# Kernel tuning notes

Measured on AMD Instinct MI355X. Metric: run time of the kernel, lower is better.

Reference implementation:

```python
import jax, jax.numpy as jnp
import numpy as np

B, S, DIM, HD = 4, 1024, 2048, 128
H = DIM // HD  # 16 heads
GN_EPS = 1e-3  # Keras GroupNormalization default epsilon


def setup_inputs() -> dict:
    key = jax.random.key(0)
    ks = jax.random.split(key, 8)
    x = jax.random.normal(ks[0], (B, S, DIM), dtype=jnp.float32)
    k = jax.random.normal(ks[1], (B, S, DIM), dtype=jnp.float32)
    v = jax.random.normal(ks[2], (B, S, DIM), dtype=jnp.float32)
    # One shared QKV projection weight per head (dict.fromkeys bug in source
    # makes Q, K, V use the SAME Dense layer). Keras Dense: y = x @ W, W:(in,out)
    Wh = jax.random.normal(ks[3], (H, HD, HD), dtype=jnp.float32) / np.sqrt(HD)
    wg_w = jax.random.normal(ks[4], (DIM, DIM), dtype=jnp.float32) / np.sqrt(DIM)
    wo_w = jax.random.normal(ks[5], (DIM, DIM), dtype=jnp.float32) / np.sqrt(DIM)
    gn_gamma = jnp.ones((DIM,), dtype=jnp.float32)
    gn_beta = jnp.zeros((DIM,), dtype=jnp.float32)
    return {"x": x, "k": k, "v": v, "Wh": Wh, "wg_w": wg_w, "wo_w": wo_w,
            "gn_gamma": gn_gamma, "gn_beta": gn_beta}


def _decay_masks(n_heads, seq_len):
    # Source: band_part(gamma**(i-j), 0, -1) then transpose ->
    # D[h, i, j] = gamma_h ** (j - i) for j <= i, else 0.
    gam = 1.0 - 2.0 ** (-5.0 - jnp.arange(n_heads, dtype=jnp.float32))  # (H,)
    idx = jnp.arange(seq_len, dtype=jnp.float32)
    expo = idx[None, :] - idx[:, None]               # (S,S): j - i
    D = jnp.where(expo[None, :, :] <= 0,
                  gam[:, None, None] ** expo[None, :, :], 0.0)  # (H,S,S)
    # TF: D /= reduce_sum(D, 1)**0.5 broadcasts row-sums along the COLUMN axis
    return D / jnp.sqrt(D.sum(axis=-1))[:, None, :]


def reference(x, k, v, Wh, wg_w, wo_w, gn_gamma, gn_beta):
    b, s, dim = x.shape
    h, hd, _ = Wh.shape
    # split last axis into contiguous per-head chunks
    xh = x.reshape(b, s, h, hd)
    kh = k.reshape(b, s, h, hd)
    vh = v.reshape(b, s, h, hd)
    # Q, K, V share the same per-head weight (faithful to dict.fromkeys)
    Q = jnp.einsum('bshd,hde->bshe', xh, Wh)
    K = jnp.einsum('bshd,hde->bshe', kh, Wh)
    V = jnp.einsum('bshd,hde->bshe', vh, Wh)
    scores = jnp.einsum('bshe,bthe->bhst', Q, K) / jnp.sqrt(jnp.float32(hd))
    Dn = _decay_masks(h, s)                          # (H,S,S)
    masked = scores * Dn[None, :, :, :]              # (B,H,S,S)
    # source reduces over axis 0 == BATCH, then abs, then clamp at 1
    A = jnp.maximum(jnp.abs(masked.sum(axis=0)), 1.0)  # (H,S,S)
    O = jnp.einsum('hst,bthe->bshe', A, V).reshape(b, s, dim)
    # GroupNormalization(groups=1): per-token layernorm over channels
    mu = O.mean(axis=-1, keepdims=True)
    var = O.var(axis=-1, keepdims=True)
    Y = (O - mu) / jnp.sqrt(var + GN_EPS) * gn_gamma + gn_beta
    W = jax.nn.relu(x @ wg_w)                        # gated branch
    return (W * Y) @ wo_w
```

## Files before the change

### kernel.cpp

```cpp
#include <hip/hip_runtime.h>
#include <math.h>

constexpr int Bc = 4, Sc = 1024, Dc = 2048, HDc = 128, Hc = 16;
constexpr int BSc = Bc * Sc;
constexpr int KQKc = Bc * HDc;
#define GN_EPS 1e-3f

typedef __bf16 bf16x8 __attribute__((ext_vector_type(8)));
typedef __bf16 bf16x4 __attribute__((ext_vector_type(4)));
typedef float f32x4 __attribute__((ext_vector_type(4)));

constexpr size_t OFF_Q   = 0;
constexpr size_t OFF_K   = OFF_Q + (size_t)Hc * Sc * KQKc / 2;
constexpr size_t OFF_VB  = OFF_K + (size_t)Hc * Sc * KQKc / 2;
constexpr size_t OFF_VT  = OFF_VB + (size_t)BSc * Dc / 2;
constexpr size_t OFF_A   = OFF_VT + (size_t)BSc * Dc / 2;
constexpr size_t OFF_O   = OFF_A + (size_t)Hc * Sc * Sc / 2;
constexpr size_t OFF_CT  = OFF_O + (size_t)BSc * Dc;
constexpr size_t OFF_PN  = OFF_CT + (size_t)Hc * Sc;
constexpr size_t OFF_XB  = OFF_PN + (size_t)Hc * Sc;
constexpr size_t OFF_WGT = OFF_XB + (size_t)BSc * Dc / 2;
constexpr size_t OFF_WOT = OFF_WGT + (size_t)Dc * Dc / 2;
constexpr size_t OFF_SUF = OFF_WOT + (size_t)Dc * Dc / 2;
constexpr size_t OFF_T   = OFF_SUF + (size_t)64 * 9 * HDc;
constexpr size_t OFF_WHT = OFF_T + (size_t)64 * 8 * HDc;
constexpr size_t OFF_KB2 = OFF_A;
constexpr size_t OFF_VB2 = OFF_A + (size_t)BSc * Dc / 2;

#define GLOAD_LDS16(gp, lp)                                               \
  __builtin_amdgcn_global_load_lds(                                       \
      (const __attribute__((address_space(1))) void*)(gp),                \
      (__attribute__((address_space(3))) void*)(lp), 16, 0, 0)


__global__ __launch_bounds__(256) void k_tables(float* __restrict__ ct,
                                                float* __restrict__ pn) {
  int idx = blockIdx.x * 256 + threadIdx.x;
  int h = idx >> 10, t = idx & 1023;
  double gamma = 1.0 - exp2(-(double)(5 + h));
  double l2g = log2(gamma);
  double r = 1.0 / gamma;
  double rowsum = (exp2(-(double)(t + 1) * l2g) - 1.0) / (r - 1.0);
  ct[idx] = (float)(exp2((double)t * l2g) / sqrt(rowsum));
  pn[idx] = (float)exp2(-(double)t * l2g);
}

__global__ __launch_bounds__(256) void k_cast83(const float* __restrict__ s0,
                                                const float* __restrict__ s1,
                                                const float* __restrict__ s2,
                                                __bf16* __restrict__ d0,
                                                __bf16* __restrict__ d1,
                                                __bf16* __restrict__ d2) {
  const int y = blockIdx.y;
  const float* src = (y == 0) ? s0 : (y == 1) ? s1 : s2;
  __bf16* dst = (y == 0) ? d0 : (y == 1) ? d1 : d2;
  size_t i = ((size_t)blockIdx.x * 256 + threadIdx.x) * 8;
  float4 a = *(const float4*)(src + i);
  float4 b = *(const float4*)(src + i + 4);
  bf16x8 o;
  o[0] = (__bf16)a.x; o[1] = (__bf16)a.y; o[2] = (__bf16)a.z; o[3] = (__bf16)a.w;
  o[4] = (__bf16)b.x; o[5] = (__bf16)b.y; o[6] = (__bf16)b.z; o[7] = (__bf16)b.w;
  *(bf16x8*)(dst + i) = o;
}

__global__ __launch_bounds__(256) void k_castT(const float* __restrict__ src,
                                               __bf16* __restrict__ dst) {
  __shared__ float t[32][33];
  const int bx = blockIdx.x, by = blockIdx.y;
  const int tid = threadIdx.x;
  const int lx = tid & 31, ly = tid >> 5;
  #pragma unroll
  for (int r = 0; r < 32; r += 8)
    t[ly + r][lx] = src[(size_t)(by * 32 + ly + r) * Dc + bx * 32 + lx];
  __syncthreads();
  #pragma unroll
  for (int r = 0; r < 32; r += 8)
    dst[(size_t)(bx * 32 + ly + r) * Dc + by * 32 + lx] = (__bf16)t[lx][ly + r];
}

__global__ __launch_bounds__(256) void k_whT(const float* __restrict__ Wh,
                                             __bf16* __restrict__ WhT) {
  __shared__ float t[32][33];
  const int h = blockIdx.z;
  const int d0 = blockIdx.x * 32, e0 = blockIdx.y * 32;
  const int tid = threadIdx.x;
  const int lx = tid & 31, ly = tid >> 5;
  #pragma unroll
  for (int r = 0; r < 32; r += 8)
    t[ly + r][lx] = Wh[(size_t)h * HDc * HDc + (d0 + ly + r) * HDc + e0 + lx];
  __syncthreads();
  #pragma unroll
  for (int r = 0; r < 32; r += 8)
    WhT[(size_t)h * HDc * HDc + (e0 + ly + r) * HDc + d0 + lx] =
        (__bf16)t[lx][ly + r];
}

__global__ __launch_bounds__(512) void k_projm(const __bf16* __restrict__ Xb,
                                               const __bf16* __restrict__ Kb2,
                                               const __bf16* __restrict__ Vb2,
                                               const __bf16* __restrict__ WhT,
                                               __bf16* __restrict__ Qo,
                                               __bf16* __restrict__ Ko,
                                               __bf16* __restrict__ Vo) {
  const int r0 = blockIdx.x * 128;
  const int h = blockIdx.y;
  const int z = blockIdx.z;
  const __bf16* src = (z == 0) ? Xb : (z == 1) ? Kb2 : Vb2;
  __shared__ __bf16 As[128 * 32];
  __shared__ __bf16 Bs[128 * 32];
  const int tid = threadIdx.x;
  const int wave = tid >> 6, lane = tid & 63;
  const int wm = (wave >> 2) * 64, wn = (wave & 3) * 32;
  const int grow = wave * 16 + (lane >> 2);
  const int gkb = ((lane & 3) ^ ((lane >> 3) & 3)) * 8;
  const int rl = lane & 15, kq = lane >> 4;
  const int sw8 = (kq ^ ((rl >> 1) & 3)) * 8;
  const int cha = wm >> 4, chb = wn >> 4;
  const __bf16* wb = WhT + (size_t)h * HDc * HDc;
  f32x4 acc[4][2] = {{}};
  for (int k0 = 0; k0 < HDc; k0 += 32) {
    GLOAD_LDS16(src + (size_t)(r0 + grow) * Dc + h * HDc + k0 + gkb,
                As + wave * 512);
    GLOAD_LDS16(wb + (size_t)grow * HDc + k0 + gkb, Bs + wave * 512);
    __syncthreads();
    bf16x8 a[4], b[2];
    #pragma unroll
    for (int i = 0; i < 4; ++i)
      a[i] = *(const bf16x8*)&As[(cha + i) * 512 + rl * 32 + sw8];
    #pragma unroll
    for (int j = 0; j < 2; ++j)
      b[j] = *(const bf16x8*)&Bs[(chb + j) * 512 + rl * 32 + sw8];
    #pragma unroll
    for (int i = 0; i < 4; ++i)
      #pragma unroll
      for (int j = 0; j < 2; ++j)
        acc[i][j] = __builtin_amdgcn_mfma_f32_16x16x32_bf16(a[i], b[j],
                                                            acc[i][j], 0, 0, 0);
    __syncthreads();
  }
  #pragma unroll
  for (int i = 0; i < 4; ++i) {
    #pragma unroll
    for (int j = 0; j < 2; ++j) {
      const int col = wn + j * 16 + rl;
      #pragma unroll
      for (int r = 0; r < 4; ++r) {
        const int row = r0 + wm + i * 16 + kq * 4 + r;
        const __bf16 v = (__bf16)acc[i][j][r];
        if (z == 2) {
          Vo[(size_t)row * Dc + h * HDc + col] = v;
        } else {
          const int s = row & 1023, bb = row >> 10;
          __bf16* dst = (z == 0) ? Qo : Ko;
          dst[((size_t)(h * Sc + s) * Bc + bb) * HDc + col] = v;
        }
      }
    }
  }
}

__global__ __launch_bounds__(256) void k_vt(const __bf16* __restrict__ VB,
                                            __bf16* __restrict__ Vt) {
  __shared__ float tl[32][33];
  const int bh = blockIdx.z, bb = bh >> 4, h = bh & 15;
  const int t0 = blockIdx.x * 32, e0 = blockIdx.y * 32;
  const int tid = threadIdx.x;
  const int lx = tid & 31, ly = tid >> 5;
  #pragma unroll
  for (int r = 0; r < 32; r += 8)
    tl[ly + r][lx] =
        (float)VB[(size_t)(bb * Sc + t0 + ly + r) * Dc + h * HDc + e0 + lx];
  __syncthreads();
  #pragma unroll
  for (int r = 0; r < 32; r += 8)
    Vt[((size_t)bh * HDc + e0 + ly + r) * Sc + t0 + lx] = (__bf16)tl[lx][ly + r];
}

__global__ __launch_bounds__(256) void k_vsum(const __bf16* __restrict__ VB,
                                              float* __restrict__ T) {
  const int jj = blockIdx.x, bh = blockIdx.y;
  const int bb = bh >> 4, h = bh & 15;
  const int tid = threadIdx.x;
  const int tp = tid >> 7, e = tid & 127;
  const __bf16* base =
      VB + (size_t)(bb * Sc + jj * 128 + tp * 64) * Dc + h * HDc + e;
  float a0 = 0.f, a1 = 0.f, a2 = 0.f, a3 = 0.f;
  float a4 = 0.f, a5 = 0.f, a6 = 0.f, a7 = 0.f;
  for (int t = 0; t < 64; t += 8) {
    a0 += (float)base[(size_t)(t + 0) * Dc];
    a1 += (float)base[(size_t)(t + 1) * Dc];
    a2 += (float)base[(size_t)(t + 2) * Dc];
    a3 += (float)base[(size_t)(t + 3) * Dc];
    a4 += (float)base[(size_t)(t + 4) * Dc];
    a5 += (float)base[(size_t)(t + 5) * Dc];
    a6 += (float)base[(size_t)(t + 6) * Dc];
    a7 += (float)base[(size_t)(t + 7) * Dc];
  }
  const float s = ((a0 + a1) + (a2 + a3)) + ((a4 + a5) + (a6 + a7));
  __shared__ float red[2][128];
  red[tp][e] = s;
  __syncthreads();
  if (tp == 0)
    T[((size_t)bh * 8 + jj) * HDc + e] = red[0][e] + red[1][e];
}

__global__ __launch_bounds__(128) void k_vscan(const float* __restrict__ T,
                                               float* __restrict__ SufV) {
  const int bh = blockIdx.x;
  const int e = threadIdx.x;
  float acc = 0.f;
  SufV[((size_t)bh * 9 + 8) * HDc + e] = 0.f;
  for (int jj = 7; jj >= 1; --jj) {
    acc += T[((size_t)bh * 8 + jj) * HDc + e];
    SufV[((size_t)bh * 9 + jj) * HDc + e] = acc;
  }
}

__global__ __launch_bounds__(512) void k_ssm(const __bf16* __restrict__ Q,
                                             const __bf16* __restrict__ Kb,
                                             const float* __restrict__ ct,
                                             const float* __restrict__ pn,
                                             __bf16* __restrict__ A) {
  const int bx = blockIdx.x, by = blockIdx.y;
  if (bx > by) return;
  const int h = blockIdx.z;
  const int t0 = bx * 128, s0 = by * 128;
  const int tid = threadIdx.x;
  __bf16* Ah = A + (size_t)h * Sc * Sc;
  __shared__ __bf16 Qs[128 * 32];
  __shared__ __bf16 Ks[128 * 32];
  const int wave = tid >> 6, lane = tid & 63;
  const int wm = (wave >> 2) * 64, wn = (wave & 3) * 32;
  const int grow = wave * 16 + (lane >> 2);
  const int gkb = ((lane & 3) ^ ((lane >> 3) & 3)) * 8;
  const int rl = lane & 15, kq = lane >> 4;
  const int sw8 = (kq ^ ((rl >> 1) & 3)) * 8;
  const int cha = wm >> 4, chb = wn >> 4;
  f32x4 acc[4][2] = {{}};
  const __bf16* qbase = Q + (size_t)(h * Sc + s0) * KQKc;
  const __bf16* kbase = Kb + (size_t)(h * Sc + t0) * KQKc;
  for (int k0 = 0; k0 < KQKc; k0 += 32) {
    GLOAD_LDS16(qbase + (size_t)grow * KQKc + k0 + gkb, Qs + wave * 512);
    GLOAD_LDS16(kbase + (size_t)grow * KQKc + k0 + gkb, Ks + wave * 512);
    __syncthreads();
    bf16x8 a[4], b[2];
    #pragma unroll
    for (int i = 0; i < 4; ++i)
      a[i] = *(const bf16x8*)&Qs[(cha + i) * 512 + rl * 32 + sw8];
    #pragma unroll
    for (int j = 0; j < 2; ++j)
      b[j] = *(const bf16x8*)&Ks[(chb + j) * 512 + rl * 32 + sw8];
    #pragma unroll
    for (int i = 0; i < 4; ++i)
      #pragma unroll
      for (int j = 0; j < 2; ++j)
        acc[i][j] = __builtin_amdgcn_mfma_f32_16x16x32_bf16(a[i], b[j],
                                                            acc[i][j], 0, 0, 0);
    __syncthreads();
  }
  const float rs = 0.088388347648318447f;
  #pragma unroll
  for (int i = 0; i < 4; ++i) {
    #pragma unroll
    for (int j = 0; j < 2; ++j) {
      const int t = t0 + wn + j * 16 + rl;
      const float ctv = ct[h * Sc + t] * rs;
      #pragma unroll
      for (int r = 0; r < 4; ++r) {
        const int s = s0 + wm + i * 16 + kq * 4 + r;
        float v = 1.0f;
        if (t <= s) v = fmaxf(fabsf(ctv * pn[h * Sc + s] * acc[i][j][r]), 1.0f);
        Ah[(size_t)s * Sc + t] = (__bf16)v;
      }
    }
  }
}

__global__ __launch_bounds__(512) void k_avm(const __bf16* __restrict__ A,
                                             const __bf16* __restrict__ Vt,
                                             const float* __restrict__ SufV,
                                             float* __restrict__ O) {
  const int bh = blockIdx.z, bb = bh >> 4, h = bh & 15;
  const int itile = blockIdx.x;
  const int s0 = itile * 128;
  const int tid = threadIdx.x;
  __shared__ __bf16 As[128 * 32];
  __shared__ __bf16 Bs[128 * 32];
  const int wave = tid >> 6, lane = tid & 63;
  const int wm = (wave >> 2) * 64, wn = (wave & 3) * 32;
  const int grow = wave * 16 + (lane >> 2);
  const int gkb = ((lane & 3) ^ ((lane >> 3) & 3)) * 8;
  const int rl = lane & 15, kq = lane >> 4;
  const int sw8 = (kq ^ ((rl >> 1) & 3)) * 8;
  const int cha = wm >> 4, chb = wn >> 4;
  f32x4 acc[4][2] = {{}};
  const __bf16* abase = A + (size_t)(h * Sc + s0) * Sc;
  const __bf16* vbase = Vt + (size_t)bh * HDc * Sc;
  const int kmax = (itile + 1) * 128;
  for (int k0 = 0; k0 < kmax; k0 += 32) {
    GLOAD_LDS16(abase + (size_t)grow * Sc + k0 + gkb, As + wave * 512);
    GLOAD_LDS16(vbase + (size_t)grow * Sc + k0 + gkb, Bs + wave * 512);
    __syncthreads();
    bf16x8 a[4], b[2];
    #pragma unroll
    for (int i = 0; i < 4; ++i)
      a[i] = *(const bf16x8*)&As[(cha + i) * 512 + rl * 32 + sw8];
    #pragma unroll
    for (int j = 0; j < 2; ++j)
      b[j] = *(const bf16x8*)&Bs[(chb + j) * 512 + rl * 32 + sw8];
    #pragma unroll
    for (int i = 0; i < 4; ++i)
      #pragma unroll
      for (int j = 0; j < 2; ++j)
        acc[i][j] = __builtin_amdgcn_mfma_f32_16x16x32_bf16(a[i], b[j],
                                                            acc[i][j], 0, 0, 0);
    __syncthreads();
  }
  const float* sufr = SufV + ((size_t)bh * 9 + (itile + 1)) * HDc;
  #pragma unroll
  for (int i = 0; i < 4; ++i) {
    #pragma unroll
    for (int j = 0; j < 2; ++j) {
      const int e = wn + j * 16 + rl;
      const float sv = sufr[e];
      #pragma unroll
      for (int r = 0; r < 4; ++r) {
        const int s = s0 + wm + i * 16 + kq * 4 + r;
        O[(size_t)(bb * Sc + s) * Dc + h * HDc + e] = acc[i][j][r] + sv;
      }
    }
  }
}

__global__ __launch_bounds__(256) void k_gnorm(float* __restrict__ O,
                                               const float* __restrict__ gw,
                                               const float* __restrict__ bw) {
  const int r = blockIdx.x;
  const int tid = threadIdx.x;
  float* row = O + (size_t)r * Dc;
  const int c = tid * 4;
  float4 v0 = *(const float4*)(row + c);
  float4 v1 = *(const float4*)(row + c + 1024);
  __shared__ float red[256];
  __shared__ float sh_mu, sh_inv;
  red[tid] = v0.x + v0.y + v0.z + v0.w + v1.x + v1.y + v1.z + v1.w;
  __syncthreads();
  for (int st = 128; st > 0; st >>= 1) {
    if (tid < st) red[tid] += red[tid + st];
    __syncthreads();
  }
  if (tid == 0) sh_mu = red[0] * (1.0f / Dc);
  __syncthreads();
  const float mu = sh_mu;
  float d[8] = {v0.x - mu, v0.y - mu, v0.z - mu, v0.w - mu,
                v1.x - mu, v1.y - mu, v1.z - mu, v1.w - mu};
  float ssq = 0.f;
  #pragma unroll
  for (int i = 0; i < 8; ++i) ssq += d[i] * d[i];
  red[tid] = ssq;
  __syncthreads();
  for (int st = 128; st > 0; st >>= 1) {
    if (tid < st) red[tid] += red[tid + st];
    __syncthreads();
  }
  if (tid == 0) sh_inv = rsqrtf(red[0] * (1.0f / Dc) + GN_EPS);
  __syncthreads();
  const float inv = sh_inv;
  float4 g0 = *(const float4*)(gw + c), g1 = *(const float4*)(gw + c + 1024);
  float4 b0 = *(const float4*)(bw + c), b1 = *(const float4*)(bw + c + 1024);
  float4 o0, o1;
  o0.x = d[0] * inv * g0.x + b0.x; o0.y = d[1] * inv * g0.y + b0.y;
  o0.z = d[2] * inv * g0.z + b0.z; o0.w = d[3] * inv * g0.w + b0.w;
  o1.x = d[4] * inv * g1.x + b1.x; o1.y = d[5] * inv * g1.y + b1.y;
  o1.z = d[6] * inv * g1.z + b1.z; o1.w = d[7] * inv * g1.w + b1.w;
  *(float4*)(row + c) = o0;
  *(float4*)(row + c + 1024) = o1;
}

constexpr int NTK = Dc / 64;
constexpr int ABUFE = 256 * 64;
constexpr int BBUFE = 128 * 64;
constexpr int MG_LDS = (3 * ABUFE + 2 * BBUFE) * 2;

__global__ __launch_bounds__(512, 2) void k_mgemm(const __bf16* __restrict__ Ab,
                                                  const __bf16* __restrict__ Bt,
                                                  const float* __restrict__ Y,
                                                  __bf16* __restrict__ Gout,
                                                  float* __restrict__ Fout,
                                                  int mode) {
  extern __shared__ __bf16 lds[];
  __bf16* As = lds;
  __bf16* Bs = lds + 3 * ABUFE;
  int wid = blockIdx.y * gridDim.x + blockIdx.x;
  wid = (wid & 7) * 32 + (wid >> 3);
  const int r0 = (wid >> 4) * 256;
  const int c0 = (wid & 15) * 128;
  const int tid = threadIdx.x;
  const int wave = tid >> 6, lane = tid & 63;
  const int wr = wave >> 1, wc = wave & 1;
  const int lr = lane >> 2;
  const int lkx = ((lane & 3) ^ ((lane >> 3) & 3)) * 8;
  const int rl = lane & 15, kq = lane >> 4;
  const int swo = rl * 32 + ((kq ^ ((rl >> 1) & 3)) * 8);
  f32x4 acc[4][4] = {{}};

#define STAGE_A_(i, kt, bsel) do {                                          \
    const int ci_ = (i) * 8 + wave;                                         \
    GLOAD_LDS16(Ab + (size_t)(r0 + (ci_ >> 1) * 16 + lr) * Dc               \
                    + (kt) * 64 + (ci_ & 1) * 32 + lkx,                     \
                As + (bsel) * ABUFE + ci_ * 512);                           \
  } while (0)
#define STAGE_B_(j, kt, bsel) do {                                          \
    const int ci_ = (j) * 8 + wave;                                         \
    GLOAD_LDS16(Bt + (size_t)(c0 + (ci_ >> 1) * 16 + lr) * Dc               \
                    + (kt) * 64 + (ci_ & 1) * 32 + lkx,                     \
                Bs + (bsel) * BBUFE + ci_ * 512);                           \
  } while (0)

  STAGE_A_(0, 0, 0); STAGE_A_(1, 0, 0); STAGE_A_(2, 0, 0); STAGE_A_(3, 0, 0);
  STAGE_B_(0, 0, 0); STAGE_B_(1, 0, 0);
  STAGE_A_(0, 1, 1); STAGE_A_(1, 1, 1); STAGE_A_(2, 1, 1); STAGE_A_(3, 1, 1);
  STAGE_B_(0, 1, 1); STAGE_B_(1, 1, 1);
  __builtin_amdgcn_sched_barrier(0);
  asm volatile("s_waitcnt vmcnt(6)" ::: "memory");
  __builtin_amdgcn_sched_barrier(0);
  __builtin_amdgcn_s_barrier();

  int cbA = 0;
  for (int t = 0; t < NTK; ++t) {
    const int sbA = (cbA + 2 >= 3) ? cbA - 1 : cbA + 2;
    const int cbB = t & 1;
    const __bf16* Ac = As + cbA * ABUFE;
    const __bf16* Bc = Bs + cbB * BBUFE;
    const bool st = (t + 2) < NTK;
    bf16x8 a01[2][2], a23[2][2], b01[2][2], b23[2][2];
    #pragma unroll
    for (int m = 0; m < 2; ++m)
      #pragma unroll
      for (int kc = 0; kc < 2; ++kc)
        a01[m][kc] = *(const bf16x8*)&Ac[((wr * 4 + m) * 2 + kc) * 512 + swo];
    #pragma unroll
    for (int n = 0; n < 2; ++n)
      #pragma unroll
      for (int kc = 0; kc < 2; ++kc)
        b01[n][kc] = *(const bf16x8*)&Bc[((wc * 4 + n) * 2 + kc) * 512 + swo];
    if (st) { STAGE_A_(0, t + 2, sbA); STAGE_A_(1, t + 2, sbA); }
    __builtin_amdgcn_sched_barrier(0);
    __builtin_amdgcn_s_barrier();
    asm volatile("s_waitcnt lgkmcnt(0)" ::: "memory");
    __builtin_amdgcn_sched_barrier(0);
    __builtin_amdgcn_s_setprio(1);
    #pragma unroll
    for (int kc = 0; kc < 2; ++kc)
      #pragma unroll
      for (int m = 0; m < 2; ++m)
        #pragma unroll
        for (int n = 0; n < 2; ++n)
          acc[m][n] = __builtin_amdgcn_mfma_f32_16x16x32_bf16(
              a01[m][kc], b01[n][kc], acc[m][n], 0, 0, 0);
    __builtin_amdgcn_s_setprio(0);
    __builtin_amdgcn_sched_barrier(0);
    __builtin_amdgcn_s_barrier();
    #pragma unroll
    for (int n = 0; n < 2; ++n)
      #pragma unroll
      for (int kc = 0; kc < 2; ++kc)
        b23[n][kc] = *(const bf16x8*)&Bc[((wc * 4 + 2 + n) * 2 + kc) * 512 + swo];
    if (st) { STAGE_A_(2, t + 2, sbA); STAGE_A_(3, t + 2, sbA); }
    __builtin_amdgcn_sched_barrier(0);
    __builtin_amdgcn_s_barrier();
    asm volatile("s_waitcnt lgkmcnt(0)" ::: "memory");
    __builtin_amdgcn_sched_barrier(0);
    __builtin_amdgcn_s_setprio(1);
    #pragma unroll
    for (int kc = 0; kc < 2; ++kc)
      #pragma unroll
      for (int m = 0; m < 2; ++m)
        #pragma unroll
        for (int n = 0; n < 2; ++n)
          acc[m][2 + n] = __builtin_amdgcn_mfma_f32_16x16x32_bf16(
              a01[m][kc], b23[n][kc], acc[m][2 + n], 0, 0, 0);
    __builtin_amdgcn_s_setprio(0);
    __builtin_amdgcn_sched_barrier(0);
    __builtin_amdgcn_s_barrier();
    #pragma unroll
    for (int m = 0; m < 2; ++m)
      #pragma unroll
      for (int kc = 0; kc < 2; ++kc)
        a23[m][kc] = *(const bf16x8*)&Ac[((wr * 4 + 2 + m) * 2 + kc) * 512 + swo];
    if (st) { STAGE_B_(0, t + 2, cbB); STAGE_B_(1, t + 2, cbB); }
    __builtin_amdgcn_sched_barrier(0);
    __builtin_amdgcn_s_barrier();
    asm volatile("s_waitcnt lgkmcnt(0)" ::: "memory");
    __builtin_amdgcn_sched_barrier(0);
    __builtin_amdgcn_s_setprio(1);
    #pragma unroll
    for (int kc = 0; kc < 2; ++kc)
      #pragma unroll
      for (int m = 0; m < 2; ++m)
        #pragma unroll
        for (int n = 0; n < 2; ++n)
          acc[2 + m][n] = __builtin_amdgcn_mfma_f32_16x16x32_bf16(
              a23[m][kc], b01[n][kc], acc[2 + m][n], 0, 0, 0);
    __builtin_amdgcn_s_setprio(0);
    __builtin_amdgcn_sched_barrier(0);
    __builtin_amdgcn_s_barrier();
    __builtin_amdgcn_sched_barrier(0);
    if (st)
      asm volatile("s_waitcnt vmcnt(6)" ::: "memory");
    else if (t + 1 < NTK)
      asm volatile("s_waitcnt vmcnt(0)" ::: "memory");
    __builtin_amdgcn_sched_barrier(0);
    __builtin_amdgcn_s_barrier();
    __builtin_amdgcn_s_setprio(1);
    #pragma unroll
    for (int kc = 0; kc < 2; ++kc)
      #pragma unroll
      for (int m = 0; m < 2; ++m)
        #pragma unroll
        for (int n = 0; n < 2; ++n)
          acc[2 + m][2 + n] = __builtin_amdgcn_mfma_f32_16x16x32_bf16(
              a23[m][kc], b23[n][kc], acc[2 + m][2 + n], 0, 0, 0);
    __builtin_amdgcn_s_setprio(0);
    __builtin_amdgcn_sched_barrier(0);
    __builtin_amdgcn_s_barrier();
    cbA = (cbA + 1 >= 3) ? 0 : cbA + 1;
  }
#undef STAGE_A_
#undef STAGE_B_

  #pragma unroll
  for (int mi = 0; mi < 4; ++mi) {
    #pragma unroll
    for (int nj = 0; nj < 4; ++nj) {
      const int col = c0 + wc * 64 + nj * 16 + rl;
      #pragma unroll
      for (int r = 0; r < 4; ++r) {
        const int row = r0 + wr * 64 + mi * 16 + kq * 4 + r;
        const size_t idx = (size_t)row * Dc + col;
        float v = acc[mi][nj][r];
        if (mode == 0) {
          v = fmaxf(v, 0.f) * Y[idx];
          Gout[idx] = (__bf16)v;
        } else {
          Fout[idx] = v;
        }
      }
    }
  }
}

extern "C" void kernel_launch(void* const* d_in, const int* in_sizes, int n_in,
                              void* d_out, int out_size, void* d_ws, size_t ws_size,
                              hipStream_t stream) {
  const float* x  = (const float*)d_in[0];
  const float* k  = (const float*)d_in[1];
  const float* v  = (const float*)d_in[2];
  const float* Wh = (const float*)d_in[3];
  const float* wg = (const float*)d_in[4];
  const float* wo = (const float*)d_in[5];
  const float* gg = (const float*)d_in[6];
  const float* gb = (const float*)d_in[7];
  float* ws = (float*)d_ws;
  __bf16* Q   = (__bf16*)(ws + OFF_Q);
  __bf16* Kp  = (__bf16*)(ws + OFF_K);
  __bf16* VB  = (__bf16*)(ws + OFF_VB);
  __bf16* Vt  = (__bf16*)(ws + OFF_VT);
  __bf16* A   = (__bf16*)(ws + OFF_A);
  float*  O   = ws + OFF_O;
  float*  CT  = ws + OFF_CT;
  float*  PN  = ws + OFF_PN;
  __bf16* XB  = (__bf16*)(ws + OFF_XB);
  __bf16* WGT = (__bf16*)(ws + OFF_WGT);
  __bf16* WOT = (__bf16*)(ws + OFF_WOT);
  float*  SUF = ws + OFF_SUF;
  float*  TP  = ws + OFF_T;
  __bf16* WHT = (__bf16*)(ws + OFF_WHT);
  __bf16* KB2 = (__bf16*)(ws + OFF_KB2);
  __bf16* VB2 = (__bf16*)(ws + OFF_VB2);
  __bf16* G   = (__bf16*)(ws + OFF_Q);

  static bool attr_done = false;
  if (!attr_done) {
    (void)hipFuncSetAttribute((const void*)k_mgemm,
                              hipFuncAttributeMaxDynamicSharedMemorySize,
                              MG_LDS);
    attr_done = true;
  }

  k_tables<<<Hc * Sc / 256, 256, 0, stream>>>(CT, PN);
  k_cast83<<<dim3((BSc * Dc) / (256 * 8), 3), 256, 0, stream>>>(
      x, k, v, XB, KB2, VB2);
  k_castT<<<dim3(Dc / 32, Dc / 32), 256, 0, stream>>>(wg, WGT);
  k_castT<<<dim3(Dc / 32, Dc / 32), 256, 0, stream>>>(wo, WOT);
  k_whT<<<dim3(4, 4, Hc), 256, 0, stream>>>(Wh, WHT);
  k_projm<<<dim3(BSc / 128, Hc, 3), 512, 0, stream>>>(XB, KB2, VB2, WHT,
                                                      Q, Kp, VB);
  k_vt<<<dim3(Sc / 32, HDc / 32, Bc * Hc), 256, 0, stream>>>(VB, Vt);
  k_vsum<<<dim3(8, Bc * Hc), 256, 0, stream>>>(VB, TP);
  k_vscan<<<Bc * Hc, 128, 0, stream>>>(TP, SUF);
  k_ssm<<<dim3(Sc / 128, Sc / 128, Hc), 512, 0, stream>>>(Q, Kp, CT, PN, A);
  k_avm<<<dim3(Sc / 128, 1, Bc * Hc), 512, 0, stream>>>(A, Vt, SUF, O);
  k_gnorm<<<BSc, 256, 0, stream>>>(O, gg, gb);
  k_mgemm<<<dim3(16, 16), 512, MG_LDS, stream>>>(XB, WGT, O, G, nullptr, 0);
  k_mgemm<<<dim3(16, 16), 512, MG_LDS, stream>>>(G, WOT, nullptr, nullptr,
                                                 (float*)d_out, 1);
}
```

Baseline: 381.3 us.

## Collapse GEMM main loop to one barrier per K-tile with single-stage B prefetch

The bf16 MFMA GEMM main loop is restructured. Each wave now loads all of its A and B LDS fragments at the start of a K-tile, then issues all 16 MFMAs in four setprio blocks, with a single barrier at the end. Before, the loop interleaved fragment loads, global-to-LDS staging and four barrier-separated MFMA quarters. The B tile prefetch distance drops from two tiles to one, while A keeps its triple buffer with distance two. This removes many s_barrier and lgkmcnt stalls per iteration, at the cost of more live fragment registers and less time to hide B global-load latency.

```diff
diff --git a/kernel.cpp b/kernel.cpp
--- a/kernel.cpp
+++ b/kernel.cpp
@@ -420,34 +420,44 @@
   STAGE_A_(0, 0, 0); STAGE_A_(1, 0, 0); STAGE_A_(2, 0, 0); STAGE_A_(3, 0, 0);
   STAGE_B_(0, 0, 0); STAGE_B_(1, 0, 0);
   STAGE_A_(0, 1, 1); STAGE_A_(1, 1, 1); STAGE_A_(2, 1, 1); STAGE_A_(3, 1, 1);
-  STAGE_B_(0, 1, 1); STAGE_B_(1, 1, 1);
   __builtin_amdgcn_sched_barrier(0);
-  asm volatile("s_waitcnt vmcnt(6)" ::: "memory");
+  asm volatile("s_waitcnt vmcnt(4)" ::: "memory");
   __builtin_amdgcn_sched_barrier(0);
   __builtin_amdgcn_s_barrier();
 
   int cbA = 0;
   for (int t = 0; t < NTK; ++t) {
     const int sbA = (cbA + 2 >= 3) ? cbA - 1 : cbA + 2;
-    const int cbB = t & 1;
     const __bf16* Ac = As + cbA * ABUFE;
-    const __bf16* Bc = Bs + cbB * BBUFE;
-    const bool st = (t + 2) < NTK;
-    bf16x8 a01[2][2], a23[2][2], b01[2][2], b23[2][2];
+    const __bf16* Bc = Bs + (t & 1) * BBUFE;
+    bf16x8 a[4][2], b[4][2];
     #pragma unroll
     for (int m = 0; m < 2; ++m)
       #pragma unroll
       for (int kc = 0; kc < 2; ++kc)
-        a01[m][kc] = *(const bf16x8*)&Ac[((wr * 4 + m) * 2 + kc) * 512 + swo];
+        a[m][kc] = *(const bf16x8*)&Ac[((wr * 4 + m) * 2 + kc) * 512 + swo];
     #pragma unroll
     for (int n = 0; n < 2; ++n)
       #pragma unroll
       for (int kc = 0; kc < 2; ++kc)
-        b01[n][kc] = *(const bf16x8*)&Bc[((wc * 4 + n) * 2 + kc) * 512 + swo];
-    if (st) { STAGE_A_(0, t + 2, sbA); STAGE_A_(1, t + 2, sbA); }
-    __builtin_amdgcn_sched_barrier(0);
-    __builtin_amdgcn_s_barrier();
-    asm volatile("s_waitcnt lgkmcnt(0)" ::: "memory");
+        b[n][kc] = *(const bf16x8*)&Bc[((wc * 4 + n) * 2 + kc) * 512 + swo];
+    #pragma unroll
+    for (int m = 2; m < 4; ++m)
+      #pragma unroll
+      for (int kc = 0; kc < 2; ++kc)
+        a[m][kc] = *(const bf16x8*)&Ac[((wr * 4 + m) * 2 + kc) * 512 + swo];
+    #pragma unroll
+    for (int n = 2; n < 4; ++n)
+      #pragma unroll
+      for (int kc = 0; kc < 2; ++kc)
+        b[n][kc] = *(const bf16x8*)&Bc[((wc * 4 + n) * 2 + kc) * 512 + swo];
+    if (t + 1 < NTK) {
+      STAGE_B_(0, t + 1, (t + 1) & 1); STAGE_B_(1, t + 1, (t + 1) & 1);
+    }
+    if (t + 2 < NTK) {
+      STAGE_A_(0, t + 2, sbA); STAGE_A_(1, t + 2, sbA);
+      STAGE_A_(2, t + 2, sbA); STAGE_A_(3, t + 2, sbA);
+    }
     __builtin_amdgcn_sched_barrier(0);
     __builtin_amdgcn_s_setprio(1);
     #pragma unroll
@@ -457,19 +467,19 @@
         #pragma unroll
         for (int n = 0; n < 2; ++n)
           acc[m][n] = __builtin_amdgcn_mfma_f32_16x16x32_bf16(
-              a01[m][kc], b01[n][kc], acc[m][n], 0, 0, 0);
+              a[m][kc], b[n][kc], acc[m][n], 0, 0, 0);
     __builtin_amdgcn_s_setprio(0);
     __builtin_amdgcn_sched_barrier(0);
-    __builtin_amdgcn_s_barrier();
-    #pragma unroll
-    for (int n = 0; n < 2; ++n)
-      #pragma unroll
-      for (int kc = 0; kc < 2; ++kc)
-        b23[n][kc] = *(const bf16x8*)&Bc[((wc * 4 + 2 + n) * 2 + kc) * 512 + swo];
-    if (st) { STAGE_A_(2, t + 2, sbA); STAGE_A_(3, t + 2, sbA); }
-    __builtin_amdgcn_sched_barrier(0);
-    __builtin_amdgcn_s_barrier();
-    asm volatile("s_waitcnt lgkmcnt(0)" ::: "memory");
+    __builtin_amdgcn_s_setprio(1);
+    #pragma unroll
+    for (int kc = 0; kc < 2; ++kc)
+      #pragma unroll
+      for (int m = 2; m < 4; ++m)
+        #pragma unroll
+        for (int n = 0; n < 2; ++n)
+          acc[m][n] = __builtin_amdgcn_mfma_f32_16x16x32_bf16(
+              a[m][kc], b[n][kc], acc[m][n], 0, 0, 0);
+    __builtin_amdgcn_s_setprio(0);
     __builtin_amdgcn_sched_barrier(0);
     __builtin_amdgcn_s_setprio(1);
     #pragma unroll
@@ -477,51 +487,28 @@
       #pragma unroll
       for (int m = 0; m < 2; ++m)
         #pragma unroll
-        for (int n = 0; n < 2; ++n)
-          acc[m][2 + n] = __builtin_amdgcn_mfma_f32_16x16x32_bf16(
-              a01[m][kc], b23[n][kc], acc[m][2 + n], 0, 0, 0);
+        for (int n = 2; n < 4; ++n)
+          acc[m][n] = __builtin_amdgcn_mfma_f32_16x16x32_bf16(
+              a[m][kc], b[n][kc], acc[m][n], 0, 0, 0);
     __builtin_amdgcn_s_setprio(0);
     __builtin_amdgcn_sched_barrier(0);
-    __builtin_amdgcn_s_barrier();
-    #pragma unroll
-    for (int m = 0; m < 2; ++m)
-      #pragma unroll
-      for (int kc = 0; kc < 2; ++kc)
-        a23[m][kc] = *(const bf16x8*)&Ac[((wr * 4 + 2 + m) * 2 + kc) * 512 + swo];
-    if (st) { STAGE_B_(0, t + 2, cbB); STAGE_B_(1, t + 2, cbB); }
-    __builtin_amdgcn_sched_barrier(0);
-    __builtin_amdgcn_s_barrier();
+    __builtin_amdgcn_s_setprio(1);
+    #pragma unroll
+    for (int kc = 0; kc < 2; ++kc)
+      #pragma unroll
+      for (int m = 2; m < 4; ++m)
+        #pragma unroll
+        for (int n = 2; n < 4; ++n)
+          acc[m][n] = __builtin_amdgcn_mfma_f32_16x16x32_bf16(
+              a[m][kc], b[n][kc], acc[m][n], 0, 0, 0);
+    __builtin_amdgcn_s_setprio(0);
+    __builtin_amdgcn_sched_barrier(0);
     asm volatile("s_waitcnt lgkmcnt(0)" ::: "memory");
     __builtin_amdgcn_sched_barrier(0);
-    __builtin_amdgcn_s_setprio(1);
-    #pragma unroll
-    for (int kc = 0; kc < 2; ++kc)
-      #pragma unroll
-      for (int m = 0; m < 2; ++m)
-        #pragma unroll
-        for (int n = 0; n < 2; ++n)
-          acc[2 + m][n] = __builtin_amdgcn_mfma_f32_16x16x32_bf16(
-              a23[m][kc], b01[n][kc], acc[2 + m][n], 0, 0, 0);
-    __builtin_amdgcn_s_setprio(0);
-    __builtin_amdgcn_sched_barrier(0);
-    __builtin_amdgcn_s_barrier();
-    __builtin_amdgcn_sched_barrier(0);
-    if (st)
-      asm volatile("s_waitcnt vmcnt(6)" ::: "memory");
+    if (t + 2 < NTK)
+      asm volatile("s_waitcnt vmcnt(4)" ::: "memory");
     else if (t + 1 < NTK)
       asm volatile("s_waitcnt vmcnt(0)" ::: "memory");
-    __builtin_amdgcn_sched_barrier(0);
-    __builtin_amdgcn_s_barrier();
-    __builtin_amdgcn_s_setprio(1);
-    #pragma unroll
-    for (int kc = 0; kc < 2; ++kc)
-      #pragma unroll
-      for (int m = 0; m < 2; ++m)
-        #pragma unroll
-        for (int n = 0; n < 2; ++n)
-          acc[2 + m][2 + n] = __builtin_amdgcn_mfma_f32_16x16x32_bf16(
-              a23[m][kc], b23[n][kc], acc[2 + m][2 + n], 0, 0, 0);
-    __builtin_amdgcn_s_setprio(0);
     __builtin_amdgcn_sched_barrier(0);
     __builtin_amdgcn_s_barrier();
     cbA = (cbA + 1 >= 3) ? 0 : cbA + 1;
```

New measurement: 378.3 us. Within noise of the previous version (-0.8%).
